# Performance work log

Measured on AMD Instinct MI355X. Metric: run time of the kernel, lower is better.

The kernel has to match this reference:

```python
import jax, jax.numpy as jnp
import numpy as np

B, N, D, H, E = 128, 256, 256, 8, 524288
RATIO = 0.5
HD = D // H
K_SEL = int(N * RATIO)  # nodes kept per graph


def setup_inputs() -> dict:
    key = jax.random.key(0)
    ks = jax.random.split(key, 12)
    embeddings = jax.random.normal(ks[0], (B, N, D), dtype=jnp.float32)
    mask = jnp.ones((B, N), dtype=bool)
    dist = jax.random.uniform(ks[1], (B, N, N), dtype=jnp.float32)
    # within-graph random edges, offset per graph
    epg = E // B
    src = jax.random.randint(ks[2], (B, epg), 0, N)
    dst = jax.random.randint(ks[3], (B, epg), 0, N)
    off = (jnp.arange(B) * N)[:, None]
    edge_index = jnp.stack([(src + off).reshape(-1), (dst + off).reshape(-1)]).astype(jnp.int64)
    batch = jnp.repeat(jnp.arange(B, dtype=jnp.int64), N)
    s = 1.0 / np.sqrt(D)
    Wq = jax.random.normal(ks[4], (D, D), jnp.float32) * s
    Wk = jax.random.normal(ks[5], (D, D), jnp.float32) * s
    Wv = jax.random.normal(ks[6], (D, D), jnp.float32) * s
    Wo = jax.random.normal(ks[7], (D, D), jnp.float32) * s
    bq = jnp.zeros((D,), jnp.float32)
    bk = jnp.zeros((D,), jnp.float32)
    bv = jnp.zeros((D,), jnp.float32)
    bo = jnp.zeros((D,), jnp.float32)
    pool_w = jax.random.normal(ks[8], (D,), jnp.float32) * s
    return dict(embeddings=embeddings, mask=mask, dist=dist, edge_index=edge_index,
                batch=batch, Wq=Wq, bq=bq, Wk=Wk, bk=bk, Wv=Wv, bv=bv, Wo=Wo, bo=bo,
                pool_w=pool_w)


def _mha(x, mask, dist, Wq, bq, Wk, bk, Wv, bv, Wo, bo):
    # x: [B,N,D]; dist used as additive attention bias; mask: [B,N] key mask
    q = (x @ Wq + bq).reshape(B, N, H, HD).transpose(0, 2, 1, 3)  # bhnd
    k = (x @ Wk + bk).reshape(B, N, H, HD).transpose(0, 2, 1, 3)
    v = (x @ Wv + bv).reshape(B, N, H, HD).transpose(0, 2, 1, 3)
    scores = jnp.einsum('bhnd,bhmd->bhnm', q, k) / jnp.sqrt(jnp.float32(HD))
    scores = scores + dist[:, None]  # broadcast bias over heads
    scores = jnp.where(mask[:, None, None, :], scores, jnp.float32(-1e9))
    attn = jax.nn.softmax(scores, axis=-1)
    out = jnp.einsum('bhnm,bhmd->bhnd', attn, v)
    out = out.transpose(0, 2, 1, 3).reshape(B, N, D)
    return out @ Wo + bo


def reference(embeddings, mask, dist, edge_index, batch, Wq, bq, Wk, bk, Wv, bv, Wo, bo, pool_w):
    encoder_result = _mha(embeddings, mask, dist, Wq, bq, Wk, bk, Wv, bv, Wo, bo)
    # encoder_result[mask] -> sparse node features; mask is all-true so shape is [B*N, D]
    x = encoder_result.reshape(B * N, D)

    # ---- TopKPooling (PyG semantics): score = x.w/||w||, keep top ceil(ratio*N)/graph ----
    score = (x @ pool_w) / jnp.linalg.norm(pool_w)          # [B*N]
    vals, idx = jax.lax.top_k(score.reshape(B, N), K_SEL)    # per-graph top-k
    perm = (idx + (jnp.arange(B) * N)[:, None]).reshape(-1)  # [B*K] global node ids
    sub_x = x[perm] * jnp.tanh(vals).reshape(-1, 1)
    sub_batch = batch[perm]

    # relabel nodes: new id = position in perm (PyG ordering); dropped -> sentinel
    n_keep = B * K_SEL
    sentinel = n_keep
    new_id = jnp.full((B * N,), sentinel, dtype=edge_index.dtype).at[perm].set(
        jnp.arange(n_keep, dtype=edge_index.dtype))
    row = new_id[edge_index[0]]
    col = new_id[edge_index[1]]
    valid = (row < sentinel) & (col < sentinel)
    row = jnp.where(valid, row, sentinel)
    col = jnp.where(valid, col, sentinel)
    # sort_edge_index: row-major sort; invalid (sentinel) edges pushed to the end
    order = jnp.argsort(row * (sentinel + 1) + col)
    sub_edge_index = jnp.stack([row, col])[:, order]
    return encoder_result, sub_x, sub_edge_index, sub_batch
```

## Files before the change

kernel.cpp:

```cpp
#include <hip/hip_runtime.h>
#include <math.h>

#define Bg   128
#define Ng   256
#define Dg   256
#define Hg   8
#define HDg  32
#define Eg   524288
#define Kg   128
#define BNg  32768
#define SENT 16384

using bf16x8 = __attribute__((ext_vector_type(8))) short;
using f32x4  = __attribute__((ext_vector_type(4))) float;

__device__ inline void split2(float x, short &h, short &l) {
    unsigned u = __float_as_uint(x);
    h = (short)(u >> 16);
    float hf = __uint_as_float(u & 0xffff0000u);
    float r = x - hf;
    l = (short)(__float_as_uint(r) >> 16);
}
__device__ inline unsigned packsplit(float x) {
    unsigned u = __float_as_uint(x);
    float hf = __uint_as_float(u & 0xffff0000u);
    float r = x - hf;
    unsigned lu = __float_as_uint(r);
    return (u >> 16) | (lu & 0xffff0000u);
}
__device__ inline unsigned pack2(short a, short b) {
    return (unsigned)(unsigned short)a | ((unsigned)(unsigned short)b << 16);
}

__global__ __launch_bounds__(256) void split_x(
    const float* __restrict__ x, short* __restrict__ xh, short* __restrict__ xl)
{
    size_t i = ((size_t)blockIdx.x * 256 + threadIdx.x) * 8;
    float4 a = *(const float4*)(x + i);
    float4 b = *(const float4*)(x + i + 4);
    float v[8] = {a.x,a.y,a.z,a.w,b.x,b.y,b.z,b.w};
    short h[8], l[8];
    #pragma unroll
    for (int j = 0; j < 8; ++j) split2(v[j], h[j], l[j]);
    uint4 uh, ul;
    uh.x = pack2(h[0],h[1]); uh.y = pack2(h[2],h[3]);
    uh.z = pack2(h[4],h[5]); uh.w = pack2(h[6],h[7]);
    ul.x = pack2(l[0],l[1]); ul.y = pack2(l[2],l[3]);
    ul.z = pack2(l[4],l[5]); ul.w = pack2(l[6],l[7]);
    *(uint4*)(xh + i) = uh;
    *(uint4*)(xl + i) = ul;
}

__global__ __launch_bounds__(256) void wprep(
    const float* __restrict__ Wq, const float* __restrict__ Wk,
    const float* __restrict__ Wv, const float* __restrict__ Wo,
    short* __restrict__ WTh, short* __restrict__ WTl)
{
    __shared__ float t[64][65];
    const int bid = blockIdx.x;
    const int mat = bid >> 4;
    const int kt = (bid >> 2) & 3, nt = bid & 3;
    const float* W = (mat==0) ? Wq : (mat==1) ? Wk : (mat==2) ? Wv : Wo;
    const int tid = threadIdx.x;
    const int r = tid >> 2, c4 = tid & 3;
    #pragma unroll
    for (int i = 0; i < 4; ++i) {
        float4 v = *(const float4*)(W + (size_t)(kt*64 + r)*256 + nt*64 + c4*16 + i*4);
        t[r][c4*16 + i*4 + 0] = v.x; t[r][c4*16 + i*4 + 1] = v.y;
        t[r][c4*16 + i*4 + 2] = v.z; t[r][c4*16 + i*4 + 3] = v.w;
    }
    __syncthreads();
    const int n = r, k0 = c4 * 16;
    short hb[16], lb[16];
    #pragma unroll
    for (int i = 0; i < 16; ++i) split2(t[k0 + i][n], hb[i], lb[i]);
    size_t base = (size_t)mat*65536 + (size_t)(nt*64 + n)*256 + kt*64 + k0;
    uint4 uh0, uh1, ul0, ul1;
    uh0.x=pack2(hb[0],hb[1]);  uh0.y=pack2(hb[2],hb[3]);  uh0.z=pack2(hb[4],hb[5]);  uh0.w=pack2(hb[6],hb[7]);
    uh1.x=pack2(hb[8],hb[9]);  uh1.y=pack2(hb[10],hb[11]);uh1.z=pack2(hb[12],hb[13]);uh1.w=pack2(hb[14],hb[15]);
    ul0.x=pack2(lb[0],lb[1]);  ul0.y=pack2(lb[2],lb[3]);  ul0.z=pack2(lb[4],lb[5]);  ul0.w=pack2(lb[6],lb[7]);
    ul1.x=pack2(lb[8],lb[9]);  ul1.y=pack2(lb[10],lb[11]);ul1.z=pack2(lb[12],lb[13]);ul1.w=pack2(lb[14],lb[15]);
    *(uint4*)&WTh[base]     = uh0; *(uint4*)&WTh[base + 8] = uh1;
    *(uint4*)&WTl[base]     = ul0; *(uint4*)&WTl[base + 8] = ul1;
}

__global__ __launch_bounds__(256) void qkv_mm(
    const short* __restrict__ xh, const short* __restrict__ xl,
    const short* __restrict__ WTh, const short* __restrict__ WTl,
    const float* __restrict__ bq, const float* __restrict__ bk, const float* __restrict__ bv,
    unsigned* __restrict__ Qp, unsigned* __restrict__ Kp, unsigned* __restrict__ Vp)
{
    const int z = blockIdx.z;
    const float* bias = (z==0) ? bq : (z==1) ? bk : bv;
    unsigned* out     = (z==0) ? Qp : (z==1) ? Kp : Vp;
    const float scale = (z==0) ? 0.17677669529663687f : 1.0f;
    const short* bth = WTh + (size_t)z * 65536;
    const short* btl = WTl + (size_t)z * 65536;
    __shared__ __align__(16) short lds[16384];
    const int tid = threadIdx.x;
    const int lane = tid & 63, w = tid >> 6;
    const int g = lane >> 4, li = lane & 15;
    const int wr = w >> 1, wc = w & 1;
    const int m0 = blockIdx.x * 128, n0 = blockIdx.y * 128;
    f32x4 acc[4][4];
    #pragma unroll
    for (int i = 0; i < 4; ++i)
        #pragma unroll
        for (int j = 0; j < 4; ++j) acc[i][j] = (f32x4){0.f,0.f,0.f,0.f};

    for (int k0 = 0; k0 < 256; k0 += 32) {
        #pragma unroll
        for (int it = 0; it < 2; ++it) {
            int chunk = it*256 + tid;
            int r = chunk >> 2, c = chunk & 3;
            size_t ga = (size_t)(m0 + r)*256 + k0 + c*8;
            size_t gb = (size_t)(n0 + r)*256 + k0 + c*8;
            uint4 vh = *(const uint4*)(xh + ga);
            uint4 vl = *(const uint4*)(xl + ga);
            uint4 wh = *(const uint4*)(bth + gb);
            uint4 wl = *(const uint4*)(btl + gb);
            *(uint4*)&lds[        chunk*8] = vh;
            *(uint4*)&lds[ 4096 + chunk*8] = vl;
            *(uint4*)&lds[ 8192 + chunk*8] = wh;
            *(uint4*)&lds[12288 + chunk*8] = wl;
        }
        __syncthreads();
        bf16x8 ah[4], al[4], bh[4], bl[4];
        #pragma unroll
        for (int i = 0; i < 4; ++i) {
            int row = wr*64 + i*16 + li;
            ah[i] = *(const bf16x8*)&lds[       row*32 + g*8];
            al[i] = *(const bf16x8*)&lds[4096 + row*32 + g*8];
        }
        #pragma unroll
        for (int j = 0; j < 4; ++j) {
            int row = wc*64 + j*16 + li;
            bh[j] = *(const bf16x8*)&lds[ 8192 + row*32 + g*8];
            bl[j] = *(const bf16x8*)&lds[12288 + row*32 + g*8];
        }
        #pragma unroll
        for (int i = 0; i < 4; ++i)
            #pragma unroll
            for (int j = 0; j < 4; ++j) {
                acc[i][j] = __builtin_amdgcn_mfma_f32_16x16x32_bf16(ah[i], bh[j], acc[i][j], 0,0,0);
                acc[i][j] = __builtin_amdgcn_mfma_f32_16x16x32_bf16(ah[i], bl[j], acc[i][j], 0,0,0);
                acc[i][j] = __builtin_amdgcn_mfma_f32_16x16x32_bf16(al[i], bh[j], acc[i][j], 0,0,0);
                acc[i][j] = __builtin_amdgcn_mfma_f32_16x16x32_bf16(al[i], bl[j], acc[i][j], 0,0,0);
            }
        __syncthreads();
    }
    #pragma unroll
    for (int i = 0; i < 4; ++i)
        #pragma unroll
        for (int j = 0; j < 4; ++j)
            #pragma unroll
            for (int r = 0; r < 4; ++r) {
                int m = m0 + wr*64 + i*16 + g*4 + r;
                int c = n0 + wc*64 + j*16 + li;
                int b = m >> 8, nn = m & 255;
                int h = c >> 5, hd = c & 31;
                float val = (acc[i][j][r] + bias[c]) * scale;
                out[((size_t)(b*Hg + h)*Ng + nn)*HDg + hd] = packsplit(val);
            }
}

__global__ __launch_bounds__(256, 2) void attn_mfma(
    const unsigned* __restrict__ Qp, const unsigned* __restrict__ Kp,
    const unsigned* __restrict__ Vp, const float* __restrict__ dist,
    unsigned* __restrict__ AOp)
{
    __shared__ short    Khi[2][32][40];
    __shared__ short    Klo[2][32][40];
    __shared__ unsigned Vt [2][32][36];
    __shared__ unsigned P32[4][64][36];

    const int i0 = blockIdx.x;
    const int xcd = i0 & 7;
    const int m_  = i0 >> 3;
    const int h   = m_ & 7;
    const int b   = (m_ >> 3) * 8 + xcd;
    const int bh  = b * 8 + h;

    const int tid = threadIdx.x;
    const int w = tid >> 6;
    const int lane = tid & 63;
    const int g = lane >> 4;
    const int li = lane & 15;
    const int q0 = w * 64;
    const int skey = tid >> 3, se0 = (tid & 7) * 4;
    const float* dall = dist + (size_t)b*Ng*Ng;

    bf16x8 qh[4], ql[4];
    #pragma unroll
    for (int tq = 0; tq < 4; ++tq) {
        const unsigned* qp = Qp + ((size_t)bh * Ng + q0 + tq*16 + li) * HDg + g*8;
        uint4 u0 = *(const uint4*)qp;
        uint4 u1 = *(const uint4*)(qp + 4);
        unsigned uu[8] = {u0.x,u0.y,u0.z,u0.w,u1.x,u1.y,u1.z,u1.w};
        #pragma unroll
        for (int j = 0; j < 8; ++j) {
            qh[tq][j] = (short)(uu[j] & 0xffff);
            ql[tq][j] = (short)(uu[j] >> 16);
        }
    }

    {
        uint4 kv = *(const uint4*)(Kp + ((size_t)bh*Ng + skey) * HDg + se0);
        uint4 vv = *(const uint4*)(Vp + ((size_t)bh*Ng + skey) * HDg + se0);
        unsigned ka[4] = {kv.x,kv.y,kv.z,kv.w};
        unsigned va[4] = {vv.x,vv.y,vv.z,vv.w};
        #pragma unroll
        for (int i = 0; i < 4; ++i) {
            Khi[0][skey][se0+i] = (short)(ka[i] & 0xffff);
            Klo[0][skey][se0+i] = (short)(ka[i] >> 16);
            Vt [0][se0+i][skey] = va[i];
        }
    }
    __syncthreads();

    f32x4 O[4][2];
    #pragma unroll
    for (int tq=0;tq<4;++tq)
        #pragma unroll
        for (int td=0;td<2;++td) O[tq][td] = (f32x4){0.f,0.f,0.f,0.f};
    float lpart[4][4] = {};

    for (int ch = 0; ch < 8; ++ch) {
        const int cur = ch & 1;
        const bool pref = (ch < 7);
        uint4 kvr, vvr;
        if (pref) {
            kvr = *(const uint4*)(Kp + ((size_t)bh*Ng + (ch+1)*32 + skey) * HDg + se0);
            vvr = *(const uint4*)(Vp + ((size_t)bh*Ng + (ch+1)*32 + skey) * HDg + se0);
        }
        f32x4 sacc[4][2];
        const float* dbase = dall + ch*32;
        #pragma unroll
        for (int tq = 0; tq < 4; ++tq)
            #pragma unroll
            for (int tc = 0; tc < 2; ++tc) {
                const float* dp = dbase + (size_t)(q0 + tq*16 + g*4)*Ng + tc*16 + li;
                f32x4 s; s[0]=dp[0]; s[1]=dp[Ng]; s[2]=dp[2*Ng]; s[3]=dp[3*Ng];
                sacc[tq][tc] = s;
            }
        bf16x8 kbh[2], kbl[2];
        #pragma unroll
        for (int tc = 0; tc < 2; ++tc) {
            kbh[tc] = *(const bf16x8*)&Khi[cur][tc*16+li][g*8];
            kbl[tc] = *(const bf16x8*)&Klo[cur][tc*16+li][g*8];
        }
        #pragma unroll
        for (int tq = 0; tq < 4; ++tq)
            #pragma unroll
            for (int tc = 0; tc < 2; ++tc) {
                sacc[tq][tc] = __builtin_amdgcn_mfma_f32_16x16x32_bf16(qh[tq], kbh[tc], sacc[tq][tc], 0,0,0);
                sacc[tq][tc] = __builtin_amdgcn_mfma_f32_16x16x32_bf16(qh[tq], kbl[tc], sacc[tq][tc], 0,0,0);
                sacc[tq][tc] = __builtin_amdgcn_mfma_f32_16x16x32_bf16(ql[tq], kbh[tc], sacc[tq][tc], 0,0,0);
                sacc[tq][tc] = __builtin_amdgcn_mfma_f32_16x16x32_bf16(ql[tq], kbl[tc], sacc[tq][tc], 0,0,0);
            }
        #pragma unroll
        for (int tq = 0; tq < 4; ++tq)
            #pragma unroll
            for (int tc = 0; tc < 2; ++tc)
                #pragma unroll
                for (int r = 0; r < 4; ++r) {
                    float p = __expf(sacc[tq][tc][r] - 16.f);
                    lpart[tq][r] += p;
                    P32[w][tq*16 + g*4 + r][tc*16 + li] = packsplit(p);
                }
        bf16x8 vbh[2], vbl[2];
        #pragma unroll
        for (int td = 0; td < 2; ++td) {
            unsigned tmp[8];
            *(uint4*)&tmp[0] = *(const uint4*)&Vt[cur][td*16+li][g*8];
            *(uint4*)&tmp[4] = *(const uint4*)&Vt[cur][td*16+li][g*8+4];
            #pragma unroll
            for (int j=0;j<8;++j){ vbh[td][j]=(short)(tmp[j]&0xffff); vbl[td][j]=(short)(tmp[j]>>16); }
        }
        #pragma unroll
        for (int tq = 0; tq < 4; ++tq) {
            unsigned tmp[8];
            *(uint4*)&tmp[0] = *(const uint4*)&P32[w][tq*16+li][g*8];
            *(uint4*)&tmp[4] = *(const uint4*)&P32[w][tq*16+li][g*8+4];
            bf16x8 ph, pl;
            #pragma unroll
            for (int j=0;j<8;++j){ ph[j]=(short)(tmp[j]&0xffff); pl[j]=(short)(tmp[j]>>16); }
            #pragma unroll
            for (int td = 0; td < 2; ++td) {
                O[tq][td] = __builtin_amdgcn_mfma_f32_16x16x32_bf16(ph, vbh[td], O[tq][td], 0,0,0);
                O[tq][td] = __builtin_amdgcn_mfma_f32_16x16x32_bf16(ph, vbl[td], O[tq][td], 0,0,0);
                O[tq][td] = __builtin_amdgcn_mfma_f32_16x16x32_bf16(pl, vbh[td], O[tq][td], 0,0,0);
                O[tq][td] = __builtin_amdgcn_mfma_f32_16x16x32_bf16(pl, vbl[td], O[tq][td], 0,0,0);
            }
        }
        if (pref) {
            const int nb = cur ^ 1;
            unsigned ka[4] = {kvr.x,kvr.y,kvr.z,kvr.w};
            unsigned va[4] = {vvr.x,vvr.y,vvr.z,vvr.w};
            #pragma unroll
            for (int i = 0; i < 4; ++i) {
                Khi[nb][skey][se0+i] = (short)(ka[i] & 0xffff);
                Klo[nb][skey][se0+i] = (short)(ka[i] >> 16);
                Vt [nb][se0+i][skey] = va[i];
            }
        }
        __syncthreads();
    }
    #pragma unroll
    for (int tq = 0; tq < 4; ++tq)
        #pragma unroll
        for (int r = 0; r < 4; ++r) {
            float s = lpart[tq][r];
            s += __shfl_xor(s, 1); s += __shfl_xor(s, 2);
            s += __shfl_xor(s, 4); s += __shfl_xor(s, 8);
            lpart[tq][r] = 1.f / s;
        }
    #pragma unroll
    for (int tq = 0; tq < 4; ++tq)
        #pragma unroll
        for (int td = 0; td < 2; ++td)
            #pragma unroll
            for (int r = 0; r < 4; ++r) {
                int q = q0 + tq*16 + g*4 + r;
                float val = O[tq][td][r] * lpart[tq][r];
                AOp[((size_t)b*Ng + q)*Dg + h*HDg + td*16 + li] = packsplit(val);
            }
}

__global__ __launch_bounds__(256) void out_mm(
    const unsigned* __restrict__ aop,
    const short* __restrict__ bth, const short* __restrict__ btl,
    const float* __restrict__ bo, float* __restrict__ enc)
{
    __shared__ __align__(16) short lds[16384];
    const int tid = threadIdx.x;
    const int lane = tid & 63, w = tid >> 6;
    const int g = lane >> 4, li = lane & 15;
    const int wr = w >> 1, wc = w & 1;
    const int m0 = blockIdx.x * 128, n0 = blockIdx.y * 128;
    f32x4 acc[4][4];
    #pragma unroll
    for (int i = 0; i < 4; ++i)
        #pragma unroll
        for (int j = 0; j < 4; ++j) acc[i][j] = (f32x4){0.f,0.f,0.f,0.f};

    for (int k0 = 0; k0 < 256; k0 += 32) {
        #pragma unroll
        for (int it = 0; it < 2; ++it) {
            int chunk = it*256 + tid;
            int r = chunk >> 2, c = chunk & 3;
            size_t ga = (size_t)(m0 + r)*256 + k0 + c*8;
            size_t gb = (size_t)(n0 + r)*256 + k0 + c*8;
            uint4 p0 = *(const uint4*)(aop + ga);
            uint4 p1 = *(const uint4*)(aop + ga + 4);
            unsigned a[8] = {p0.x,p0.y,p0.z,p0.w,p1.x,p1.y,p1.z,p1.w};
            uint4 hw, lw;
            hw.x = (a[0]&0xffffu)|(a[1]<<16); lw.x = (a[0]>>16)|(a[1]&0xffff0000u);
            hw.y = (a[2]&0xffffu)|(a[3]<<16); lw.y = (a[2]>>16)|(a[3]&0xffff0000u);
            hw.z = (a[4]&0xffffu)|(a[5]<<16); lw.z = (a[4]>>16)|(a[5]&0xffff0000u);
            hw.w = (a[6]&0xffffu)|(a[7]<<16); lw.w = (a[6]>>16)|(a[7]&0xffff0000u);
            uint4 wh = *(const uint4*)(bth + gb);
            uint4 wl = *(const uint4*)(btl + gb);
            *(uint4*)&lds[        chunk*8] = hw;
            *(uint4*)&lds[ 4096 + chunk*8] = lw;
            *(uint4*)&lds[ 8192 + chunk*8] = wh;
            *(uint4*)&lds[12288 + chunk*8] = wl;
        }
        __syncthreads();
        bf16x8 ah[4], al[4], bh[4], bl[4];
        #pragma unroll
        for (int i = 0; i < 4; ++i) {
            int row = wr*64 + i*16 + li;
            ah[i] = *(const bf16x8*)&lds[       row*32 + g*8];
            al[i] = *(const bf16x8*)&lds[4096 + row*32 + g*8];
        }
        #pragma unroll
        for (int j = 0; j < 4; ++j) {
            int row = wc*64 + j*16 + li;
            bh[j] = *(const bf16x8*)&lds[ 8192 + row*32 + g*8];
            bl[j] = *(const bf16x8*)&lds[12288 + row*32 + g*8];
        }
        #pragma unroll
        for (int i = 0; i < 4; ++i)
            #pragma unroll
            for (int j = 0; j < 4; ++j) {
                acc[i][j] = __builtin_amdgcn_mfma_f32_16x16x32_bf16(ah[i], bh[j], acc[i][j], 0,0,0);
                acc[i][j] = __builtin_amdgcn_mfma_f32_16x16x32_bf16(ah[i], bl[j], acc[i][j], 0,0,0);
                acc[i][j] = __builtin_amdgcn_mfma_f32_16x16x32_bf16(al[i], bh[j], acc[i][j], 0,0,0);
                acc[i][j] = __builtin_amdgcn_mfma_f32_16x16x32_bf16(al[i], bl[j], acc[i][j], 0,0,0);
            }
        __syncthreads();
    }
    #pragma unroll
    for (int i = 0; i < 4; ++i)
        #pragma unroll
        for (int j = 0; j < 4; ++j)
            #pragma unroll
            for (int r = 0; r < 4; ++r) {
                int m = m0 + wr*64 + i*16 + g*4 + r;
                int c = n0 + wc*64 + j*16 + li;
                enc[(size_t)m*Dg + c] = acc[i][j][r] + bo[c];
            }
}

__global__ __launch_bounds__(256) void score_kernel(
    const float* __restrict__ enc, const float* __restrict__ pw, float* __restrict__ score)
{
    int row  = blockIdx.x * 8 + (threadIdx.x >> 5);
    int lane = threadIdx.x & 31;
    const float* r = enc + (size_t)row * Dg;
    float s = 0.f;
    for (int d = lane; d < Dg; d += 32) s = fmaf(r[d], pw[d], s);
    #pragma unroll
    for (int off = 16; off > 0; off >>= 1) s += __shfl_xor(s, off);
    if (lane == 0) score[row] = s;
}

__global__ void norm_kernel(const float* __restrict__ pw, float* __restrict__ inv_norm)
{
    int t = threadIdx.x;
    float s = 0.f;
    for (int d = t; d < Dg; d += 64) s = fmaf(pw[d], pw[d], s);
    #pragma unroll
    for (int off = 32; off > 0; off >>= 1) s += __shfl_xor(s, off);
    if (t == 0) *inv_norm = 1.0f / sqrtf(s);
}

__global__ __launch_bounds__(256) void topk_kernel(
    const float* __restrict__ score, float* __restrict__ vals, int* __restrict__ idxs,
    int* __restrict__ new_id, float* __restrict__ out_batch)
{
    __shared__ float sh[Ng];
    int bgr = blockIdx.x, t = threadIdx.x;
    float mine = score[(size_t)bgr * Ng + t];
    sh[t] = mine;
    __syncthreads();
    int cnt = 0;
    for (int j = 0; j < Ng; ++j) {
        float v = sh[j];
        cnt += (v > mine || (v == mine && j < t)) ? 1 : 0;
    }
    if (cnt < Kg) {
        int pos = bgr * Kg + cnt;
        vals[pos] = mine;
        idxs[pos] = t;
        new_id[bgr * Ng + t] = pos;
        out_batch[pos] = (float)bgr;
    } else {
        new_id[bgr * Ng + t] = SENT;
    }
}

__global__ __launch_bounds__(256) void subx_kernel(
    const float* __restrict__ enc, const float* __restrict__ vals,
    const int* __restrict__ idxs, const float* __restrict__ inv_norm,
    float* __restrict__ out_subx)
{
    int j    = blockIdx.x * 4 + (threadIdx.x >> 6);
    int lane = threadIdx.x & 63;
    int bgr  = j >> 7;
    int src  = bgr * Ng + idxs[j];
    float scale = tanhf(vals[j] * (*inv_norm));
    float4 v = reinterpret_cast<const float4*>(enc + (size_t)src * Dg)[lane];
    v.x *= scale; v.y *= scale; v.z *= scale; v.w *= scale;
    reinterpret_cast<float4*>(out_subx + (size_t)j * Dg)[lane] = v;
}

__global__ __launch_bounds__(256) void edge_hist(
    const int* __restrict__ ei, const int* __restrict__ new_id, int* __restrict__ counts)
{
    int e = blockIdx.x * 256 + threadIdx.x;
    int r = new_id[ei[e]];
    int c = new_id[ei[Eg + e]];
    if (r != SENT && c != SENT) atomicAdd(&counts[r], 1);
}

__global__ __launch_bounds__(256) void scan_kernel(
    const int* __restrict__ counts, int* __restrict__ offsets)
{
    __shared__ int sums[256];
    int t = threadIdx.x;
    int base = t * 64;
    int s = 0;
    for (int i = 0; i < 64; ++i) s += counts[base + i];
    sums[t] = s;
    __syncthreads();
    for (int off = 1; off < 256; off <<= 1) {
        int add = (t >= off) ? sums[t - off] : 0;
        __syncthreads();
        sums[t] += add;
        __syncthreads();
    }
    int run = sums[t] - s;
    for (int i = 0; i < 64; ++i) { offsets[base + i] = run; run += counts[base + i]; }
    if (t == 255) offsets[SENT] = run;
}

__global__ __launch_bounds__(256) void edge_scatter(
    const int* __restrict__ ei, const int* __restrict__ new_id,
    const int* __restrict__ offsets, int* __restrict__ cursor, int* __restrict__ bucket)
{
    int e = blockIdx.x * 256 + threadIdx.x;
    int r = new_id[ei[e]];
    int c = new_id[ei[Eg + e]];
    if (r != SENT && c != SENT) {
        int pos = offsets[r] + atomicAdd(&cursor[r], 1);
        bucket[pos] = c;
    }
}

__global__ __launch_bounds__(256) void edge_sort_emit(
    const int* __restrict__ offsets, int* bucket, float* __restrict__ out_edges)
{
    int r = blockIdx.x * 256 + threadIdx.x;
    int s = offsets[r], e = offsets[r + 1];
    for (int i = s + 1; i < e; ++i) {
        int key = bucket[i];
        int j = i - 1;
        while (j >= s && bucket[j] > key) { bucket[j+1] = bucket[j]; --j; }
        bucket[j+1] = key;
    }
    float rf = (float)r;
    for (int i = s; i < e; ++i) {
        out_edges[i]      = rf;
        out_edges[Eg + i] = (float)bucket[i];
    }
}

__global__ __launch_bounds__(256) void edge_fill(
    const int* __restrict__ offsets, float* __restrict__ out_edges)
{
    int p = blockIdx.x * 256 + threadIdx.x;
    if (p >= offsets[SENT]) {
        out_edges[p]      = (float)SENT;
        out_edges[Eg + p] = (float)SENT;
    }
}

extern "C" void kernel_launch(void* const* d_in, const int* in_sizes, int n_in,
                              void* d_out, int out_size, void* d_ws, size_t ws_size,
                              hipStream_t stream)
{
    const float* x    = (const float*)d_in[0];
    const float* dist = (const float*)d_in[2];
    const int*   ei   = (const int*)d_in[3];
    const float* Wq = (const float*)d_in[5];
    const float* bq = (const float*)d_in[6];
    const float* Wk = (const float*)d_in[7];
    const float* bk = (const float*)d_in[8];
    const float* Wv = (const float*)d_in[9];
    const float* bv = (const float*)d_in[10];
    const float* Wo = (const float*)d_in[11];
    const float* bo = (const float*)d_in[12];
    const float* pw = (const float*)d_in[13];

    float* out       = (float*)d_out;
    float* enc_out   = out;
    float* subx_out  = out + 8388608;
    float* edge_out  = out + 12582912;
    float* batch_out = out + 13631488;

    float* ws      = (float*)d_ws;
    unsigned* Qp   = (unsigned*)ws;
    unsigned* Kp   = (unsigned*)(ws + 8388608);
    unsigned* Vp   = (unsigned*)(ws + 16777216);
    short* xh      = (short*)(ws + 25165824);
    short* xl      = (short*)(ws + 29360128);
    unsigned* AOp  = (unsigned*)xh;
    short* WTh     = (short*)(ws + 33554432);
    short* WTl     = (short*)(ws + 33685504);
    float* score   = ws + 33816576;
    float* vals    = ws + 33849344;
    int*   idxs    = (int*)(ws + 33865728);
    int*   new_id  = (int*)(ws + 33882112);
    int*   counts  = (int*)(ws + 33914880);
    int*   offsets = (int*)(ws + 33931264);
    int*   cursor  = (int*)(ws + 33947680);
    float* inv_nm  = ws + 33964064;
    int*   bucket  = (int*)(ws + 33964096);

    hipMemsetAsync(counts, 0, SENT * sizeof(int), stream);
    hipMemsetAsync(cursor, 0, SENT * sizeof(int), stream);

    split_x       <<<dim3(4096),               256, 0, stream>>>(x, xh, xl);
    wprep         <<<dim3(64),                 256, 0, stream>>>(Wq, Wk, Wv, Wo, WTh, WTl);
    norm_kernel   <<<dim3(1),                   64, 0, stream>>>(pw, inv_nm);
    qkv_mm        <<<dim3(BNg/128, Dg/128, 3), 256, 0, stream>>>(xh, xl, WTh, WTl, bq, bk, bv, Qp, Kp, Vp);
    attn_mfma     <<<dim3(Bg*Hg),              256, 0, stream>>>(Qp, Kp, Vp, dist, AOp);
    out_mm        <<<dim3(BNg/128, Dg/128),    256, 0, stream>>>(AOp, WTh + 3*65536, WTl + 3*65536, bo, enc_out);
    score_kernel  <<<dim3(BNg/8),              256, 0, stream>>>(enc_out, pw, score);
    topk_kernel   <<<dim3(Bg),                 256, 0, stream>>>(score, vals, idxs, new_id, batch_out);
    subx_kernel   <<<dim3((Bg*Kg)/4),          256, 0, stream>>>(enc_out, vals, idxs, inv_nm, subx_out);
    edge_hist     <<<dim3(Eg/256),             256, 0, stream>>>(ei, new_id, counts);
    scan_kernel   <<<dim3(1),                  256, 0, stream>>>(counts, offsets);
    edge_scatter  <<<dim3(Eg/256),             256, 0, stream>>>(ei, new_id, offsets, cursor, bucket);
    edge_sort_emit<<<dim3(SENT/256),           256, 0, stream>>>(offsets, bucket, edge_out);
    edge_fill     <<<dim3(Eg/256),             256, 0, stream>>>(offsets, edge_out);
    (void)in_sizes; (void)n_in; (void)out_size; (void)ws_size;
}
```

Baseline: 237.4 us.

## Transpose attention MFMA operands, swizzle LDS, and vectorize dist loads and stores

Swaps the A/B operands of both attention MFMAs so each lane holds four consecutive keys or head-dims for one query row. This lets the dist bias be read as float4, P be written to LDS as uint4, and the output be stored as uint4. The padded LDS tiles for V and P are replaced with XOR-swizzled unpadded layouts, and the row-sum reduction needs fewer shuffles. Occupancy is raised to three blocks per CU, which may add register pressure or spills.

Result: slower. 242.8 us (+2.3%).

```diff
diff --git a/kernel.cpp b/kernel.cpp
--- a/kernel.cpp
+++ b/kernel.cpp
@@ -164,15 +164,15 @@
             }
 }
 
-__global__ __launch_bounds__(256, 2) void attn_mfma(
+__global__ __launch_bounds__(256, 3) void attn_mfma(
     const unsigned* __restrict__ Qp, const unsigned* __restrict__ Kp,
     const unsigned* __restrict__ Vp, const float* __restrict__ dist,
     unsigned* __restrict__ AOp)
 {
     __shared__ short    Khi[2][32][40];
     __shared__ short    Klo[2][32][40];
-    __shared__ unsigned Vt [2][32][36];
-    __shared__ unsigned P32[4][64][36];
+    __shared__ unsigned Vt [2][32][32];
+    __shared__ unsigned P32[4][64][32];
 
     const int i0 = blockIdx.x;
     const int xcd = i0 & 7;
@@ -186,6 +186,7 @@
     const int lane = tid & 63;
     const int g = lane >> 4;
     const int li = lane & 15;
+    const int r7 = li & 7;
     const int q0 = w * 64;
     const int skey = tid >> 3, se0 = (tid & 7) * 4;
     const float* dall = dist + (size_t)b*Ng*Ng;
@@ -213,7 +214,9 @@
         for (int i = 0; i < 4; ++i) {
             Khi[0][skey][se0+i] = (short)(ka[i] & 0xffff);
             Klo[0][skey][se0+i] = (short)(ka[i] >> 16);
-            Vt [0][se0+i][skey] = va[i];
+            int row = se0 + i;
+            int cs = ((((skey>>2) ^ (row&7)) << 2) | (skey&3));
+            Vt[0][row][cs] = va[i];
         }
     }
     __syncthreads();
@@ -223,7 +226,7 @@
     for (int tq=0;tq<4;++tq)
         #pragma unroll
         for (int td=0;td<2;++td) O[tq][td] = (f32x4){0.f,0.f,0.f,0.f};
-    float lpart[4][4] = {};
+    float lpart[4] = {0.f, 0.f, 0.f, 0.f};
 
     for (int ch = 0; ch < 8; ++ch) {
         const int cur = ch & 1;
@@ -234,14 +237,13 @@
             vvr = *(const uint4*)(Vp + ((size_t)bh*Ng + (ch+1)*32 + skey) * HDg + se0);
         }
         f32x4 sacc[4][2];
-        const float* dbase = dall + ch*32;
         #pragma unroll
         for (int tq = 0; tq < 4; ++tq)
             #pragma unroll
             for (int tc = 0; tc < 2; ++tc) {
-                const float* dp = dbase + (size_t)(q0 + tq*16 + g*4)*Ng + tc*16 + li;
-                f32x4 s; s[0]=dp[0]; s[1]=dp[Ng]; s[2]=dp[2*Ng]; s[3]=dp[3*Ng];
-                sacc[tq][tc] = s;
+                const float* dp = dall + (size_t)(q0 + tq*16 + li)*Ng + ch*32 + tc*16 + g*4;
+                float4 dv = *(const float4*)dp;
+                sacc[tq][tc] = (f32x4){dv.x, dv.y, dv.z, dv.w};
             }
         bf16x8 kbh[2], kbl[2];
         #pragma unroll
@@ -253,44 +255,49 @@
         for (int tq = 0; tq < 4; ++tq)
             #pragma unroll
             for (int tc = 0; tc < 2; ++tc) {
-                sacc[tq][tc] = __builtin_amdgcn_mfma_f32_16x16x32_bf16(qh[tq], kbh[tc], sacc[tq][tc], 0,0,0);
-                sacc[tq][tc] = __builtin_amdgcn_mfma_f32_16x16x32_bf16(qh[tq], kbl[tc], sacc[tq][tc], 0,0,0);
-                sacc[tq][tc] = __builtin_amdgcn_mfma_f32_16x16x32_bf16(ql[tq], kbh[tc], sacc[tq][tc], 0,0,0);
-                sacc[tq][tc] = __builtin_amdgcn_mfma_f32_16x16x32_bf16(ql[tq], kbl[tc], sacc[tq][tc], 0,0,0);
+                sacc[tq][tc] = __builtin_amdgcn_mfma_f32_16x16x32_bf16(kbh[tc], qh[tq], sacc[tq][tc], 0,0,0);
+                sacc[tq][tc] = __builtin_amdgcn_mfma_f32_16x16x32_bf16(kbl[tc], qh[tq], sacc[tq][tc], 0,0,0);
+                sacc[tq][tc] = __builtin_amdgcn_mfma_f32_16x16x32_bf16(kbh[tc], ql[tq], sacc[tq][tc], 0,0,0);
+                sacc[tq][tc] = __builtin_amdgcn_mfma_f32_16x16x32_bf16(kbl[tc], ql[tq], sacc[tq][tc], 0,0,0);
             }
         #pragma unroll
         for (int tq = 0; tq < 4; ++tq)
             #pragma unroll
-            for (int tc = 0; tc < 2; ++tc)
-                #pragma unroll
-                for (int r = 0; r < 4; ++r) {
-                    float p = __expf(sacc[tq][tc][r] - 16.f);
-                    lpart[tq][r] += p;
-                    P32[w][tq*16 + g*4 + r][tc*16 + li] = packsplit(p);
-                }
+            for (int tc = 0; tc < 2; ++tc) {
+                float p0 = __expf(sacc[tq][tc][0] - 16.f);
+                float p1 = __expf(sacc[tq][tc][1] - 16.f);
+                float p2 = __expf(sacc[tq][tc][2] - 16.f);
+                float p3 = __expf(sacc[tq][tc][3] - 16.f);
+                lpart[tq] += p0; lpart[tq] += p1; lpart[tq] += p2; lpart[tq] += p3;
+                uint4 pw4;
+                pw4.x = packsplit(p0); pw4.y = packsplit(p1);
+                pw4.z = packsplit(p2); pw4.w = packsplit(p3);
+                int slot = (4*tc + g) ^ r7;
+                *(uint4*)&P32[w][tq*16 + li][slot << 2] = pw4;
+            }
         bf16x8 vbh[2], vbl[2];
         #pragma unroll
         for (int td = 0; td < 2; ++td) {
             unsigned tmp[8];
-            *(uint4*)&tmp[0] = *(const uint4*)&Vt[cur][td*16+li][g*8];
-            *(uint4*)&tmp[4] = *(const uint4*)&Vt[cur][td*16+li][g*8+4];
+            *(uint4*)&tmp[0] = *(const uint4*)&Vt[cur][td*16+li][((2*g  ) ^ r7) << 2];
+            *(uint4*)&tmp[4] = *(const uint4*)&Vt[cur][td*16+li][((2*g+1) ^ r7) << 2];
             #pragma unroll
             for (int j=0;j<8;++j){ vbh[td][j]=(short)(tmp[j]&0xffff); vbl[td][j]=(short)(tmp[j]>>16); }
         }
         #pragma unroll
         for (int tq = 0; tq < 4; ++tq) {
             unsigned tmp[8];
-            *(uint4*)&tmp[0] = *(const uint4*)&P32[w][tq*16+li][g*8];
-            *(uint4*)&tmp[4] = *(const uint4*)&P32[w][tq*16+li][g*8+4];
+            *(uint4*)&tmp[0] = *(const uint4*)&P32[w][tq*16+li][((2*g  ) ^ r7) << 2];
+            *(uint4*)&tmp[4] = *(const uint4*)&P32[w][tq*16+li][((2*g+1) ^ r7) << 2];
             bf16x8 ph, pl;
             #pragma unroll
             for (int j=0;j<8;++j){ ph[j]=(short)(tmp[j]&0xffff); pl[j]=(short)(tmp[j]>>16); }
             #pragma unroll
             for (int td = 0; td < 2; ++td) {
-                O[tq][td] = __builtin_amdgcn_mfma_f32_16x16x32_bf16(ph, vbh[td], O[tq][td], 0,0,0);
-                O[tq][td] = __builtin_amdgcn_mfma_f32_16x16x32_bf16(ph, vbl[td], O[tq][td], 0,0,0);
-                O[tq][td] = __builtin_amdgcn_mfma_f32_16x16x32_bf16(pl, vbh[td], O[tq][td], 0,0,0);
-                O[tq][td] = __builtin_amdgcn_mfma_f32_16x16x32_bf16(pl, vbl[td], O[tq][td], 0,0,0);
+                O[tq][td] = __builtin_amdgcn_mfma_f32_16x16x32_bf16(vbh[td], ph, O[tq][td], 0,0,0);
+                O[tq][td] = __builtin_amdgcn_mfma_f32_16x16x32_bf16(vbl[td], ph, O[tq][td], 0,0,0);
+                O[tq][td] = __builtin_amdgcn_mfma_f32_16x16x32_bf16(vbh[td], pl, O[tq][td], 0,0,0);
+                O[tq][td] = __builtin_amdgcn_mfma_f32_16x16x32_bf16(vbl[td], pl, O[tq][td], 0,0,0);
             }
         }
         if (pref) {
@@ -301,30 +308,34 @@
             for (int i = 0; i < 4; ++i) {
                 Khi[nb][skey][se0+i] = (short)(ka[i] & 0xffff);
                 Klo[nb][skey][se0+i] = (short)(ka[i] >> 16);
-                Vt [nb][se0+i][skey] = va[i];
+                int row = se0 + i;
+                int cs = ((((skey>>2) ^ (row&7)) << 2) | (skey&3));
+                Vt[nb][row][cs] = va[i];
             }
         }
         __syncthreads();
     }
+    float inv[4];
+    #pragma unroll
+    for (int tq = 0; tq < 4; ++tq) {
+        float s = lpart[tq];
+        s += __shfl_xor(s, 16);
+        s += __shfl_xor(s, 32);
+        inv[tq] = 1.f / s;
+    }
     #pragma unroll
     for (int tq = 0; tq < 4; ++tq)
         #pragma unroll
-        for (int r = 0; r < 4; ++r) {
-            float s = lpart[tq][r];
-            s += __shfl_xor(s, 1); s += __shfl_xor(s, 2);
-            s += __shfl_xor(s, 4); s += __shfl_xor(s, 8);
-            lpart[tq][r] = 1.f / s;
-        }
-    #pragma unroll
-    for (int tq = 0; tq < 4; ++tq)
-        #pragma unroll
-        for (int td = 0; td < 2; ++td)
-            #pragma unroll
-            for (int r = 0; r < 4; ++r) {
-                int q = q0 + tq*16 + g*4 + r;
-                float val = O[tq][td][r] * lpart[tq][r];
-                AOp[((size_t)b*Ng + q)*Dg + h*HDg + td*16 + li] = packsplit(val);
-            }
+        for (int td = 0; td < 2; ++td) {
+            uint4 o4;
+            o4.x = packsplit(O[tq][td][0] * inv[tq]);
+            o4.y = packsplit(O[tq][td][1] * inv[tq]);
+            o4.z = packsplit(O[tq][td][2] * inv[tq]);
+            o4.w = packsplit(O[tq][td][3] * inv[tq]);
+            int q = q0 + tq*16 + li;
+            int d = h*HDg + td*16 + g*4;
+            *(uint4*)&AOp[((size_t)b*Ng + q)*Dg + d] = o4;
+        }
 }
 
 __global__ __launch_bounds__(256) void out_mm(
```
